# Kernel tuning notes

Hardware: AMD Instinct MI355X
Metric: run time of the kernel (lower is better)

## Reference

```python
import jax, jax.numpy as jnp
import numpy as np
from jax import lax

T = 8192
OBS = 512
HID = 2048
NOBJ = 8


def setup_inputs() -> dict:
    key = jax.random.key(0)
    ks = jax.random.split(key, 9)
    s_in = 1.0 / np.sqrt(OBS)
    s_hid = 1.0 / np.sqrt(HID)
    return {
        "x": jax.random.normal(ks[0], (T, OBS), dtype=jnp.float32),
        "W_in": jax.random.normal(ks[1], (HID, OBS), dtype=jnp.float32) * s_in,
        "W_B": jax.random.normal(ks[2], (HID, OBS), dtype=jnp.float32) * s_in,
        "W_C": jax.random.normal(ks[3], (HID, OBS), dtype=jnp.float32) * s_in,
        "W_delta": jax.random.normal(ks[4], (HID, OBS), dtype=jnp.float32) * s_in,
        "A_log": jax.random.normal(ks[5], (HID,), dtype=jnp.float32),
        "W_out": jax.random.normal(ks[6], (NOBJ, HID), dtype=jnp.float32) * s_hid,
        "b_out": jnp.zeros((NOBJ,), dtype=jnp.float32),
        "W_skip": jax.random.normal(ks[7], (NOBJ, OBS), dtype=jnp.float32) * s_in,
    }


def reference(x, W_in, W_B, W_C, W_delta, A_log, W_out, b_out, W_skip):
    # Input-dependent SSM parameters (4 GEMMs, [T, HID] each)
    x_state = x @ W_in.T
    B = x @ W_B.T
    C = x @ W_C.T
    delta = jax.nn.sigmoid(x @ W_delta.T)
    A = -jnp.exp(A_log)                      # [HID]

    A_bar = jnp.exp(delta * A)               # [T, HID], per-step decay
    Bx = B * x_state                         # [T, HID], per-step input

    def step(h, inp):
        a, bx = inp
        h = a * h + bx
        return h, h

    h0 = jnp.zeros((HID,), dtype=x.dtype)
    _, h_seq = lax.scan(step, h0, (A_bar, Bx))  # [T, HID]

    y = C * h_seq
    out = y @ W_out.T + b_out + x @ W_skip.T    # [T, NOBJ]
    return out
```

## Files before the change

kernel.cpp:

```cpp
#include <hip/hip_runtime.h>
#include <hip/hip_bf16.h>
#include <cstdint>

#define TT   8192
#define KOBS 512
#define HID  2048
#define NOBJ 8
#define NCH  64
#define CT   128

typedef unsigned short u16;
typedef short bf16x8 __attribute__((ext_vector_type(8)));
typedef float f32x4  __attribute__((ext_vector_type(4)));
typedef unsigned short u16x4 __attribute__((ext_vector_type(4)));

static __device__ __forceinline__ float bf2f(u16 u) {
    union { uint32_t i; float f; } v;
    v.i = ((uint32_t)u) << 16;
    return v.f;
}
static __device__ __forceinline__ u16 f2bf(float f) {
    union { float f; uint32_t i; } v;
    v.f = f;
    uint32_t lsb = (v.i >> 16) & 1u;
    uint32_t r = v.i + 0x7fffu + lsb;
    return (u16)(r >> 16);
}

static __device__ __forceinline__ void async_ld16(const u16* g, u16* l) {
    __builtin_amdgcn_global_load_lds(
        (const __attribute__((address_space(1))) uint32_t*)g,
        (__attribute__((address_space(3))) uint32_t*)l,
        16, 0, 0);
}

__global__ void prep_kernel(const float* __restrict__ x,
                            const float* __restrict__ Win,
                            const float* __restrict__ WB,
                            const float* __restrict__ WC,
                            const float* __restrict__ Wd,
                            const float* __restrict__ A_log,
                            u16* __restrict__ x_bf,
                            u16* __restrict__ W_bf,
                            float* __restrict__ A_e)
{
    const int64_t NX = (int64_t)TT * KOBS;
    const int64_t NW = (int64_t)4 * HID * KOBS;
    int64_t i = (int64_t)blockIdx.x * blockDim.x + threadIdx.x;
    int64_t stride = (int64_t)gridDim.x * blockDim.x;

    for (int64_t t = i; t < NX; t += stride) x_bf[t] = f2bf(x[t]);

    for (int64_t t = i; t < NW; t += stride) {
        int n = (int)(t >> 9);
        int k = (int)(t & 511);
        int h = n >> 2;
        int w = n & 3;
        const float* src = (w == 0) ? Win : (w == 1) ? WB : (w == 2) ? WC : Wd;
        W_bf[t] = f2bf(src[(int64_t)h * KOBS + k]);
    }

    for (int64_t t = i; t < HID; t += stride)
        A_e[t] = -__expf(A_log[t]) * 1.44269504f;
}

__launch_bounds__(256)
__global__ void gemm_fused(const u16* __restrict__ x_bf,
                           const u16* __restrict__ W_bf,
                           const float* __restrict__ A_e,
                           u16* __restrict__ BX,
                           u16* __restrict__ CC,
                           u16* __restrict__ LA,
                           float* __restrict__ P,
                           float* __restrict__ S)
{
    __shared__ __align__(16) u16 smem[3 * 128 * 40];
    __shared__ float Ps[256], Ss[256];
    u16* a_s = smem;
    u16* b_s = smem + 4096;

    const int tid  = threadIdx.x;
    const int bm   = blockIdx.x & 63;
    const int bn   = blockIdx.x >> 6;
    const int m0t  = bm * 128;
    const int n0   = bn * 128;
    const int lane = tid & 63;
    const int wave = tid >> 6;
    const int wn   = (wave & 1) * 64;
    const int wt   = (wave >> 1) * 64;
    const int fr   = lane & 15;
    const int fq   = lane >> 4;

    f32x4 acc[4][4];
#pragma unroll
    for (int i = 0; i < 4; i++)
#pragma unroll
        for (int j = 0; j < 4; j++) {
            f32x4 z = {0.f, 0.f, 0.f, 0.f};
            acc[i][j] = z;
        }

    const int srow = tid >> 2;
    const int scg  = (tid & 3) ^ ((srow >> 1) & 3);
    const u16* gA0 = x_bf + (size_t)(m0t + srow) * KOBS + scg * 8;
    const u16* gA1 = gA0 + (size_t)64 * KOBS;
    const u16* gB0 = W_bf + (size_t)(n0 + srow) * KOBS + scg * 8;
    const u16* gB1 = gB0 + (size_t)64 * KOBS;
    u16* lA0 = &a_s[tid * 8];
    u16* lA1 = &a_s[2048 + tid * 8];
    u16* lB0 = &b_s[tid * 8];
    u16* lB1 = &b_s[2048 + tid * 8];

    const int pcg = fq ^ ((fr >> 1) & 3);

    for (int kb = 0; kb < KOBS; kb += 32) {
        async_ld16(gA0 + kb, lA0);
        async_ld16(gA1 + kb, lA1);
        async_ld16(gB0 + kb, lB0);
        async_ld16(gB1 + kb, lB1);
        __syncthreads();

        bf16x8 af[4], bfx[4];
#pragma unroll
        for (int i = 0; i < 4; i++)
            af[i] = *(const bf16x8*)&b_s[(wn + i * 16 + fr) * 32 + pcg * 8];
#pragma unroll
        for (int j = 0; j < 4; j++)
            bfx[j] = *(const bf16x8*)&a_s[(wt + j * 16 + fr) * 32 + pcg * 8];

#pragma unroll
        for (int i = 0; i < 4; i++)
#pragma unroll
            for (int j = 0; j < 4; j++)
                acc[i][j] = __builtin_amdgcn_mfma_f32_16x16x32_bf16(
                    af[i], bfx[j], acc[i][j], 0, 0, 0);
        __syncthreads();
    }

    const int hq = wn >> 2;
#pragma unroll
    for (int i = 0; i < 4; i++) {
        const int hl = hq + i * 4 + fq;
        const float ae = A_e[bn * 32 + hl];
#pragma unroll
        for (int j = 0; j < 4; j++) {
            const int tl = wt + j * 16 + fr;
            f32x4 v = acc[i][j];
            float sig = 1.0f / (1.0f + __expf(-v[3]));
            smem[(0 * 128 + tl) * 40 + hl] = f2bf(v[0] * v[1]);
            smem[(1 * 128 + tl) * 40 + hl] = f2bf(v[2]);
            smem[(2 * 128 + tl) * 40 + hl] = f2bf(sig * ae);
        }
    }
    __syncthreads();

#pragma unroll
    for (int it = 0; it < 6; it++) {
        const int g = it * 64 + (tid >> 2);
        const int a = g >> 7;
        const int t = g & 127;
        const int c = tid & 3;
        uint4 vd = *(const uint4*)&smem[(a * 128 + t) * 40 + c * 8];
        u16* dst = (a == 0 ? BX : (a == 1 ? CC : LA)) +
                   (size_t)(m0t + t) * HID + bn * 32 + c * 8;
        *(uint4*)dst = vd;
    }

    {
        const int hi  = tid & 31;
        const int seg = tid >> 5;
        float p = 1.f, s = 0.f;
        const int tbase = seg * 16;
#pragma unroll
        for (int t = 0; t < 16; t++) {
            float a  = exp2f(bf2f(smem[(2 * 128 + tbase + t) * 40 + hi]));
            float bx = bf2f(smem[(0 * 128 + tbase + t) * 40 + hi]);
            s = fmaf(a, s, bx);
            p *= a;
        }
        Ps[seg * 32 + hi] = p;
        Ss[seg * 32 + hi] = s;
        __syncthreads();
        if (tid < 32) {
            float pt = 1.f, st = 0.f;
#pragma unroll
            for (int sg = 0; sg < 8; sg++) {
                float ps = Ps[sg * 32 + tid], ss = Ss[sg * 32 + tid];
                st = fmaf(ps, st, ss);
                pt *= ps;
            }
            P[(size_t)bm * HID + bn * 32 + tid] = pt;
            S[(size_t)bm * HID + bn * 32 + tid] = st;
        }
    }
}

__global__ void scan_combine(const float* __restrict__ P,
                             const float* __restrict__ S,
                             float* __restrict__ H0)
{
    const int h = blockIdx.x * 256 + threadIdx.x;
    float hrun = 0.f;
    for (int c = 0; c < NCH; c++) {
        H0[c * HID + h] = hrun;
        hrun = fmaf(P[c * HID + h], hrun, S[c * HID + h]);
    }
}

__global__ void scan_pass2(const u16* __restrict__ LA,
                           const u16* __restrict__ BX,
                           const u16* __restrict__ CC,
                           const float* __restrict__ H0,
                           u16* __restrict__ Y)
{
    const int c = blockIdx.x >> 3;
    const int h = ((blockIdx.x & 7) << 8) + threadIdx.x;
    float hrun = H0[c * HID + h];
    size_t base = (size_t)c * CT * HID + h;
    for (int t = 0; t < CT; t++) {
        float a  = exp2f(bf2f(LA[base]));
        float bx = bf2f(BX[base]);
        hrun = fmaf(a, hrun, bx);
        Y[base] = f2bf(bf2f(CC[base]) * hrun);
        base += HID;
    }
}

__launch_bounds__(256)
__global__ void out_kernel(const u16* __restrict__ Y,
                           const float* __restrict__ x,
                           const float* __restrict__ W_out,
                           const float* __restrict__ b_out,
                           const float* __restrict__ W_skip,
                           float* __restrict__ out)
{
    const int wave = threadIdx.x >> 6;
    const int lane = threadIdx.x & 63;
    const int t0 = (blockIdx.x * 4 + wave) * 4;

    float acc[4][NOBJ];
#pragma unroll
    for (int tt = 0; tt < 4; tt++)
#pragma unroll
        for (int o = 0; o < NOBJ; o++) acc[tt][o] = 0.f;

#pragma unroll 2
    for (int i = 0; i < 8; i++) {
        const int hv = (i * 64 + lane) * 4;
        float4 w[NOBJ];
#pragma unroll
        for (int o = 0; o < NOBJ; o++)
            w[o] = *(const float4*)(W_out + (size_t)o * HID + hv);
#pragma unroll
        for (int tt = 0; tt < 4; tt++) {
            u16x4 yv = *(const u16x4*)(Y + (size_t)(t0 + tt) * HID + hv);
            float y0 = bf2f(yv[0]), y1 = bf2f(yv[1]);
            float y2 = bf2f(yv[2]), y3 = bf2f(yv[3]);
#pragma unroll
            for (int o = 0; o < NOBJ; o++)
                acc[tt][o] += y0 * w[o].x + y1 * w[o].y +
                              y2 * w[o].z + y3 * w[o].w;
        }
    }
#pragma unroll
    for (int i = 0; i < 2; i++) {
        const int kv = (i * 64 + lane) * 4;
        float4 w[NOBJ];
#pragma unroll
        for (int o = 0; o < NOBJ; o++)
            w[o] = *(const float4*)(W_skip + (size_t)o * KOBS + kv);
#pragma unroll
        for (int tt = 0; tt < 4; tt++) {
            float4 xv = *(const float4*)(x + (size_t)(t0 + tt) * KOBS + kv);
#pragma unroll
            for (int o = 0; o < NOBJ; o++)
                acc[tt][o] += xv.x * w[o].x + xv.y * w[o].y +
                              xv.z * w[o].z + xv.w * w[o].w;
        }
    }

#pragma unroll
    for (int s = 32; s > 0; s >>= 1)
#pragma unroll
        for (int tt = 0; tt < 4; tt++)
#pragma unroll
            for (int o = 0; o < NOBJ; o++)
                acc[tt][o] += __shfl_xor(acc[tt][o], s, 64);

    if (lane == 0) {
#pragma unroll
        for (int tt = 0; tt < 4; tt++)
#pragma unroll
            for (int o = 0; o < NOBJ; o++)
                out[(size_t)(t0 + tt) * NOBJ + o] = acc[tt][o] + b_out[o];
    }
}

extern "C" void kernel_launch(void* const* d_in, const int* in_sizes, int n_in,
                              void* d_out, int out_size, void* d_ws, size_t ws_size,
                              hipStream_t stream)
{
    const float* x      = (const float*)d_in[0];
    const float* Win    = (const float*)d_in[1];
    const float* WB     = (const float*)d_in[2];
    const float* WC     = (const float*)d_in[3];
    const float* Wd     = (const float*)d_in[4];
    const float* A_log  = (const float*)d_in[5];
    const float* W_out  = (const float*)d_in[6];
    const float* b_out  = (const float*)d_in[7];
    const float* W_skip = (const float*)d_in[8];
    float* out = (float*)d_out;

    char* ws = (char*)d_ws;
    size_t off = 0;
    auto alloc = [&](size_t bytes) -> void* {
        void* p = (void*)(ws + off);
        off += (bytes + 255) & ~(size_t)255;
        return p;
    };

    u16*   x_bf = (u16*)  alloc((size_t)TT * KOBS * 2);
    u16*   W_bf = (u16*)  alloc((size_t)4 * HID * KOBS * 2);
    float* A_e  = (float*)alloc((size_t)HID * 4);
    u16*   LA   = (u16*)  alloc((size_t)TT * HID * 2);
    u16*   BX   = (u16*)  alloc((size_t)TT * HID * 2);
    u16*   CC   = (u16*)  alloc((size_t)TT * HID * 2);
    float* P    = (float*)alloc((size_t)NCH * HID * 4);
    float* S    = (float*)alloc((size_t)NCH * HID * 4);
    float* H0   = (float*)alloc((size_t)NCH * HID * 4);
    u16*   Y    = (u16*)  alloc((size_t)TT * HID * 2);
    (void)ws_size; (void)in_sizes; (void)n_in; (void)out_size;

    prep_kernel<<<2048, 256, 0, stream>>>(x, Win, WB, WC, Wd, A_log,
                                          x_bf, W_bf, A_e);
    gemm_fused<<<4096, 256, 0, stream>>>(x_bf, W_bf, A_e, BX, CC, LA, P, S);
    scan_combine<<<8, 256, 0, stream>>>(P, S, H0);
    scan_pass2<<<512, 256, 0, stream>>>(LA, BX, CC, H0, Y);
    out_kernel<<<512, 256, 0, stream>>>(Y, x, W_out, b_out, W_skip, out);
}
```

Measured before the change: 236.3 us.

## Fuse scan pass with output projection via MFMA and interleave LA/BX storage

```diff
diff --git a/kernel.cpp b/kernel.cpp
--- a/kernel.cpp
+++ b/kernel.cpp
@@ -10,9 +10,9 @@
 #define CT   128
 
 typedef unsigned short u16;
+typedef uint32_t u32;
 typedef short bf16x8 __attribute__((ext_vector_type(8)));
 typedef float f32x4  __attribute__((ext_vector_type(4)));
-typedef unsigned short u16x4 __attribute__((ext_vector_type(4)));
 
 static __device__ __forceinline__ float bf2f(u16 u) {
     union { uint32_t i; float f; } v;
@@ -65,19 +65,68 @@
 }
 
 __launch_bounds__(256)
+__global__ void init_out(const float* __restrict__ x,
+                         const float* __restrict__ b_out,
+                         const float* __restrict__ W_skip,
+                         float* __restrict__ out)
+{
+    const int wave = threadIdx.x >> 6;
+    const int lane = threadIdx.x & 63;
+    const int t0 = (blockIdx.x * 4 + wave) * 4;
+
+    float acc[4][NOBJ];
+#pragma unroll
+    for (int tt = 0; tt < 4; tt++)
+#pragma unroll
+        for (int o = 0; o < NOBJ; o++) acc[tt][o] = 0.f;
+
+#pragma unroll
+    for (int i = 0; i < 2; i++) {
+        const int kv = (i * 64 + lane) * 4;
+        float4 w[NOBJ];
+#pragma unroll
+        for (int o = 0; o < NOBJ; o++)
+            w[o] = *(const float4*)(W_skip + (size_t)o * KOBS + kv);
+#pragma unroll
+        for (int tt = 0; tt < 4; tt++) {
+            float4 xv = *(const float4*)(x + (size_t)(t0 + tt) * KOBS + kv);
+#pragma unroll
+            for (int o = 0; o < NOBJ; o++)
+                acc[tt][o] += xv.x * w[o].x + xv.y * w[o].y +
+                              xv.z * w[o].z + xv.w * w[o].w;
+        }
+    }
+#pragma unroll
+    for (int s = 32; s > 0; s >>= 1)
+#pragma unroll
+        for (int tt = 0; tt < 4; tt++)
+#pragma unroll
+            for (int o = 0; o < NOBJ; o++)
+                acc[tt][o] += __shfl_xor(acc[tt][o], s, 64);
+    if (lane == 0) {
+#pragma unroll
+        for (int tt = 0; tt < 4; tt++)
+#pragma unroll
+            for (int o = 0; o < NOBJ; o++)
+                out[(size_t)(t0 + tt) * NOBJ + o] = acc[tt][o] + b_out[o];
+    }
+}
+
+__launch_bounds__(256)
 __global__ void gemm_fused(const u16* __restrict__ x_bf,
                            const u16* __restrict__ W_bf,
                            const float* __restrict__ A_e,
-                           u16* __restrict__ BX,
-                           u16* __restrict__ CC,
-                           u16* __restrict__ LA,
+                           u32* __restrict__ LABX,
+                           u16* __restrict__ CCg,
                            float* __restrict__ P,
                            float* __restrict__ S)
 {
-    __shared__ __align__(16) u16 smem[3 * 128 * 40];
+    __shared__ __align__(16) u32 smem32[7168];
     __shared__ float Ps[256], Ss[256];
-    u16* a_s = smem;
-    u16* b_s = smem + 4096;
+    u16* a_s = (u16*)smem32;
+    u16* b_s = a_s + 4096;
+    u32* epL = smem32;
+    u16* epC = (u16*)(smem32 + 4608);
 
     const int tid  = threadIdx.x;
     const int bm   = blockIdx.x & 63;
@@ -146,24 +195,27 @@
         for (int j = 0; j < 4; j++) {
             const int tl = wt + j * 16 + fr;
             f32x4 v = acc[i][j];
+            float bx = v[0] * v[1];
             float sig = 1.0f / (1.0f + __expf(-v[3]));
-            smem[(0 * 128 + tl) * 40 + hl] = f2bf(v[0] * v[1]);
-            smem[(1 * 128 + tl) * 40 + hl] = f2bf(v[2]);
-            smem[(2 * 128 + tl) * 40 + hl] = f2bf(sig * ae);
+            epL[tl * 36 + hl] = ((u32)f2bf(sig * ae) << 16) | (u32)f2bf(bx);
+            epC[tl * 40 + hl] = f2bf(v[2]);
         }
     }
     __syncthreads();
 
 #pragma unroll
-    for (int it = 0; it < 6; it++) {
-        const int g = it * 64 + (tid >> 2);
-        const int a = g >> 7;
-        const int t = g & 127;
-        const int c = tid & 3;
-        uint4 vd = *(const uint4*)&smem[(a * 128 + t) * 40 + c * 8];
-        u16* dst = (a == 0 ? BX : (a == 1 ? CC : LA)) +
-                   (size_t)(m0t + t) * HID + bn * 32 + c * 8;
-        *(uint4*)dst = vd;
+    for (int it = 0; it < 4; it++) {
+        const int g = it * 256 + tid;
+        const int row = g >> 3, cs = g & 7;
+        uint4 v = *(const uint4*)&epL[row * 36 + cs * 4];
+        *(uint4*)(LABX + (size_t)(m0t + row) * HID + bn * 32 + cs * 4) = v;
+    }
+#pragma unroll
+    for (int it = 0; it < 2; it++) {
+        const int g = it * 256 + tid;
+        const int row = g >> 2, cs = g & 3;
+        uint4 v = *(const uint4*)&epC[row * 40 + cs * 8];
+        *(uint4*)(CCg + (size_t)(m0t + row) * HID + bn * 32 + cs * 8) = v;
     }
 
     {
@@ -173,8 +225,9 @@
         const int tbase = seg * 16;
 #pragma unroll
         for (int t = 0; t < 16; t++) {
-            float a  = exp2f(bf2f(smem[(2 * 128 + tbase + t) * 40 + hi]));
-            float bx = bf2f(smem[(0 * 128 + tbase + t) * 40 + hi]);
+            u32 w = epL[(tbase + t) * 36 + hi];
+            float a  = exp2f(bf2f((u16)(w >> 16)));
+            float bx = bf2f((u16)(w & 0xffff));
             s = fmaf(a, s, bx);
             p *= a;
         }
@@ -207,92 +260,70 @@
     }
 }
 
-__global__ void scan_pass2(const u16* __restrict__ LA,
-                           const u16* __restrict__ BX,
-                           const u16* __restrict__ CC,
-                           const float* __restrict__ H0,
-                           u16* __restrict__ Y)
-{
-    const int c = blockIdx.x >> 3;
-    const int h = ((blockIdx.x & 7) << 8) + threadIdx.x;
+__launch_bounds__(256)
+__global__ void scan_out(const u32* __restrict__ LABX,
+                         const u16* __restrict__ CCg,
+                         const float* __restrict__ H0,
+                         const float* __restrict__ W_out,
+                         float* __restrict__ out)
+{
+    __shared__ __align__(16) u16 ybuf[128 * 256];
+    const int tid  = threadIdx.x;
+    const int c    = blockIdx.x >> 3;
+    const int hg   = blockIdx.x & 7;
+    const int lane = tid & 63;
+    const int wave = tid >> 6;
+    const int fr   = lane & 15;
+    const int fq   = lane >> 4;
+
+    bf16x8 bw[8];
+#pragma unroll
+    for (int ks = 0; ks < 8; ks++) {
+        bf16x8 w;
+#pragma unroll
+        for (int j = 0; j < 8; j++) {
+            const int hb = hg * 256 + ks * 32 + fq * 8 + j;
+            u16 v = (fr < 8) ? f2bf(W_out[(size_t)fr * HID + hb]) : (u16)0;
+            w[j] = (short)v;
+        }
+        bw[ks] = w;
+    }
+
+    const int h = hg * 256 + tid;
     float hrun = H0[c * HID + h];
-    size_t base = (size_t)c * CT * HID + h;
+    size_t base = ((size_t)c * CT) * HID + h;
+    const int g  = tid >> 3;
+    const int lo = tid & 7;
     for (int t = 0; t < CT; t++) {
-        float a  = exp2f(bf2f(LA[base]));
-        float bx = bf2f(BX[base]);
+        u32 wv   = LABX[base];
+        float bx = bf2f((u16)(wv & 0xffff));
+        float a  = exp2f(bf2f((u16)(wv >> 16)));
+        float cc = bf2f(CCg[base]);
         hrun = fmaf(a, hrun, bx);
-        Y[base] = f2bf(bf2f(CC[base]) * hrun);
+        ybuf[t * 256 + (((g ^ (t & 7)) << 3) | lo)] = f2bf(cc * hrun);
         base += HID;
     }
-}
-
-__launch_bounds__(256)
-__global__ void out_kernel(const u16* __restrict__ Y,
-                           const float* __restrict__ x,
-                           const float* __restrict__ W_out,
-                           const float* __restrict__ b_out,
-                           const float* __restrict__ W_skip,
-                           float* __restrict__ out)
-{
-    const int wave = threadIdx.x >> 6;
-    const int lane = threadIdx.x & 63;
-    const int t0 = (blockIdx.x * 4 + wave) * 4;
-
-    float acc[4][NOBJ];
-#pragma unroll
-    for (int tt = 0; tt < 4; tt++)
-#pragma unroll
-        for (int o = 0; o < NOBJ; o++) acc[tt][o] = 0.f;
-
-#pragma unroll 2
-    for (int i = 0; i < 8; i++) {
-        const int hv = (i * 64 + lane) * 4;
-        float4 w[NOBJ];
-#pragma unroll
-        for (int o = 0; o < NOBJ; o++)
-            w[o] = *(const float4*)(W_out + (size_t)o * HID + hv);
-#pragma unroll
-        for (int tt = 0; tt < 4; tt++) {
-            u16x4 yv = *(const u16x4*)(Y + (size_t)(t0 + tt) * HID + hv);
-            float y0 = bf2f(yv[0]), y1 = bf2f(yv[1]);
-            float y2 = bf2f(yv[2]), y3 = bf2f(yv[3]);
-#pragma unroll
-            for (int o = 0; o < NOBJ; o++)
-                acc[tt][o] += y0 * w[o].x + y1 * w[o].y +
-                              y2 * w[o].z + y3 * w[o].w;
-        }
-    }
-#pragma unroll
-    for (int i = 0; i < 2; i++) {
-        const int kv = (i * 64 + lane) * 4;
-        float4 w[NOBJ];
-#pragma unroll
-        for (int o = 0; o < NOBJ; o++)
-            w[o] = *(const float4*)(W_skip + (size_t)o * KOBS + kv);
-#pragma unroll
-        for (int tt = 0; tt < 4; tt++) {
-            float4 xv = *(const float4*)(x + (size_t)(t0 + tt) * KOBS + kv);
-#pragma unroll
-            for (int o = 0; o < NOBJ; o++)
-                acc[tt][o] += xv.x * w[o].x + xv.y * w[o].y +
-                              xv.z * w[o].z + xv.w * w[o].w;
-        }
-    }
-
-#pragma unroll
-    for (int s = 32; s > 0; s >>= 1)
-#pragma unroll
-        for (int tt = 0; tt < 4; tt++)
-#pragma unroll
-            for (int o = 0; o < NOBJ; o++)
-                acc[tt][o] += __shfl_xor(acc[tt][o], s, 64);
-
-    if (lane == 0) {
-#pragma unroll
-        for (int tt = 0; tt < 4; tt++)
-#pragma unroll
-            for (int o = 0; o < NOBJ; o++)
-                out[(size_t)(t0 + tt) * NOBJ + o] = acc[tt][o] + b_out[o];
+    __syncthreads();
+
+#pragma unroll
+    for (int mt = 0; mt < 2; mt++) {
+        const int tb = wave * 32 + mt * 16;
+        const int t  = tb + fr;
+        f32x4 acc2 = {0.f, 0.f, 0.f, 0.f};
+#pragma unroll
+        for (int ks = 0; ks < 8; ks++) {
+            const int gg = ks * 4 + fq;
+            bf16x8 yv = *(const bf16x8*)
+                &ybuf[t * 256 + ((gg ^ (fr & 7)) << 3)];
+            acc2 = __builtin_amdgcn_mfma_f32_16x16x32_bf16(bw[ks], yv, acc2,
+                                                           0, 0, 0);
+        }
+        if (fq < 2) {
+            const int tg = c * CT + tb + fr;
+#pragma unroll
+            for (int reg = 0; reg < 4; reg++)
+                atomicAdd(&out[(size_t)tg * NOBJ + 4 * fq + reg], acc2[reg]);
+        }
     }
 }
 
@@ -322,19 +353,17 @@
     u16*   x_bf = (u16*)  alloc((size_t)TT * KOBS * 2);
     u16*   W_bf = (u16*)  alloc((size_t)4 * HID * KOBS * 2);
     float* A_e  = (float*)alloc((size_t)HID * 4);
-    u16*   LA   = (u16*)  alloc((size_t)TT * HID * 2);
-    u16*   BX   = (u16*)  alloc((size_t)TT * HID * 2);
-    u16*   CC   = (u16*)  alloc((size_t)TT * HID * 2);
+    u32*   LABX = (u32*)  alloc((size_t)TT * HID * 4);
+    u16*   CCg  = (u16*)  alloc((size_t)TT * HID * 2);
     float* P    = (float*)alloc((size_t)NCH * HID * 4);
     float* S    = (float*)alloc((size_t)NCH * HID * 4);
     float* H0   = (float*)alloc((size_t)NCH * HID * 4);
-    u16*   Y    = (u16*)  alloc((size_t)TT * HID * 2);
     (void)ws_size; (void)in_sizes; (void)n_in; (void)out_size;
 
     prep_kernel<<<2048, 256, 0, stream>>>(x, Win, WB, WC, Wd, A_log,
                                           x_bf, W_bf, A_e);
-    gemm_fused<<<4096, 256, 0, stream>>>(x_bf, W_bf, A_e, BX, CC, LA, P, S);
+    init_out<<<512, 256, 0, stream>>>(x, b_out, W_skip, out);
+    gemm_fused<<<4096, 256, 0, stream>>>(x_bf, W_bf, A_e, LABX, CCg, P, S);
     scan_combine<<<8, 256, 0, stream>>>(P, S, H0);
-    scan_pass2<<<512, 256, 0, stream>>>(LA, BX, CC, H0, Y);
-    out_kernel<<<512, 256, 0, stream>>>(Y, x, W_out, b_out, W_skip, out);
-}
+    scan_out<<<512, 256, 0, stream>>>(LABX, CCg, H0, W_out, out);
+}
```

Result: slower. 242.7 us (+2.7%).
